# Performance work log

Hardware: AMD Instinct MI355X
Metric: run time of the kernel (lower is better)

## Reference

```python
import jax, jax.numpy as jnp
import numpy as np

B, S, HID = 4, 1024, 1024
NH, HD = 16, 64  # num heads, head dim


def setup_inputs() -> dict:
    key = jax.random.key(0)
    ks = jax.random.split(key, 8)
    scale = 0.02
    return {
        "hidden_states": jax.random.normal(ks[0], (B, S, HID), dtype=jnp.float32),
        "attention_mask": jnp.ones((B, 1, 1, S), dtype=jnp.float32),
        "Wq": jax.random.normal(ks[1], (HID, HID), dtype=jnp.float32) * scale,
        "bq": jnp.zeros((HID,), dtype=jnp.float32),
        "Wk": jax.random.normal(ks[2], (HID, HID), dtype=jnp.float32) * scale,
        "bk": jnp.zeros((HID,), dtype=jnp.float32),
        "Wv": jax.random.normal(ks[3], (HID, HID), dtype=jnp.float32) * scale,
        "bv": jnp.zeros((HID,), dtype=jnp.float32),
    }


def reference(hidden_states, attention_mask, Wq, bq, Wk, bk, Wv, bv):
    # Linear projections: torch nn.Linear computes x @ W.T + b
    q = hidden_states @ Wq.T + bq  # [B,S,HID]
    k = hidden_states @ Wk.T + bk
    v = hidden_states @ Wv.T + bv

    def split_heads(x):
        return x.reshape(B, S, NH, HD).transpose(0, 2, 1, 3)  # [B,NH,S,HD]

    q, k, v = split_heads(q), split_heads(k), split_heads(v)

    scores = jnp.einsum("bhqd,bhkd->bhqk", q, k) / jnp.sqrt(jnp.float32(HD))
    # faithful to original: scores - (2 - mask) * 1e6
    scores = scores - (2.0 - attention_mask) * 1.0e6
    probs = jax.nn.softmax(scores, axis=-1)
    # dropout: eval mode -> identity
    ctx = jnp.einsum("bhqk,bhkd->bhqd", probs, v)  # [B,NH,S,HD]
    ctx = ctx.transpose(0, 2, 1, 3).reshape(B, S, HID)
    return ctx
```

## Files before the change

### kernel.cpp

```cpp
#include <hip/hip_runtime.h>
#include <math.h>

#define B_ 4
#define S_ 1024
#define HID_ 1024
#define NH_ 16
#define HD_ 64
#define NTOK (B_ * S_)

typedef __attribute__((ext_vector_type(4))) float f32x4;
typedef __attribute__((ext_vector_type(16))) float f32x16;
typedef __attribute__((ext_vector_type(8))) short bf16x8;

__device__ __forceinline__ unsigned short f2bf(float f) {
    union { float f; unsigned int u; } v; v.f = f;
    unsigned int r = v.u + 0x7fffu + ((v.u >> 16) & 1u);
    return (unsigned short)(r >> 16);
}

#if __has_builtin(__builtin_amdgcn_cvt_pk_bf16_f32)
__device__ __forceinline__ unsigned int pk_bf16(float a, float b) {
    auto v = __builtin_amdgcn_cvt_pk_bf16_f32(a, b);
    union { decltype(v) v; unsigned int u; } cv; cv.v = v;
    return cv.u;
}
#else
__device__ __forceinline__ unsigned int pk_bf16(float a, float b) {
    return (unsigned int)f2bf(a) | ((unsigned int)f2bf(b) << 16);
}
#endif

#if __has_builtin(__builtin_amdgcn_permlane32_swap)
__device__ __forceinline__ void plswap(unsigned &a, unsigned &b) {
    typedef __attribute__((ext_vector_type(2))) int v2i;
    v2i r = __builtin_amdgcn_permlane32_swap((int)a, (int)b, false, false);
    a = (unsigned)r[0]; b = (unsigned)r[1];
}
#else
__device__ __forceinline__ void plswap(unsigned &a, unsigned &b) {
    const unsigned bl = __shfl_xor(b, 32);
    const unsigned ah = __shfl_xor(a, 32);
    const bool hi = ((threadIdx.x & 63) >> 5) != 0;
    const unsigned na = hi ? bl : a;
    const unsigned nb = hi ? b  : ah;
    a = na; b = nb;
}
#endif

__device__ __forceinline__ void load_lds16(const void* g, void* l) {
    __builtin_amdgcn_global_load_lds(
        (const __attribute__((address_space(1))) unsigned int*)(uintptr_t)g,
        (__attribute__((address_space(3))) unsigned int*)(uintptr_t)l,
        16, 0, 0);
}

__global__ __launch_bounds__(256) void cvt_all(
    const float* __restrict__ x, const float* __restrict__ wq,
    const float* __restrict__ wk, const float* __restrict__ wv,
    unsigned short* __restrict__ xb, unsigned short* __restrict__ wqb,
    unsigned short* __restrict__ wkb, unsigned short* __restrict__ wvb)
{
    const int which = blockIdx.y;
    const float* src = which == 0 ? x : which == 1 ? wq : which == 2 ? wk : wv;
    unsigned short* dst = which == 0 ? xb : which == 1 ? wqb : which == 2 ? wkb : wvb;
    const int n4 = (which == 0) ? (NTOK * HID_ / 4) : (HID_ * HID_ / 4);
    int i = blockIdx.x * 256 + threadIdx.x;
    if (i < n4) {
        float4 f = ((const float4*)src)[i];
        uint2 o;
        o.x = pk_bf16(f.x, f.y);
        o.y = pk_bf16(f.z, f.w);
        ((uint2*)dst)[i] = o;
    }
}

__global__ __launch_bounds__(512, 6) void qkv_gemm_mfma(
    const unsigned short* __restrict__ xb,
    const unsigned short* __restrict__ Wqb, const float* __restrict__ bq,
    const unsigned short* __restrict__ Wkb, const float* __restrict__ bk,
    const unsigned short* __restrict__ Wvb, const float* __restrict__ bv,
    unsigned short* __restrict__ qout, unsigned short* __restrict__ kout,
    unsigned short* __restrict__ vtout)
{
    const int which = blockIdx.z;
    const unsigned short* __restrict__ W = which == 0 ? Wqb : which == 1 ? Wkb : Wvb;
    const float* __restrict__ bias       = which == 0 ? bq  : which == 1 ? bk  : bv;

    __shared__ unsigned short As[128 * 64];
    __shared__ unsigned short Bs[128 * 64];

    const int t    = threadIdx.x;
    const int lane = t & 63;
    const int w    = t >> 6;
    const int wr   = w >> 2;
    const int wc   = w & 3;
    const int g    = lane >> 4;
    const int lrow = lane & 15;

    const int bm = blockIdx.x;
    const int bn = blockIdx.y;

    const unsigned short* __restrict__ Arow = (which == 2) ? W  : xb;
    const unsigned short* __restrict__ Brow = (which == 2) ? xb : W;
    const int am0 = (which == 2) ? bn * 128 : bm * 128;
    const int bn0 = (which == 2) ? bm * 128 : bn * 128;

    const int srow = t >> 3;
    const int sc   = ((t & 7) ^ ((t >> 3) & 7)) << 3;
    const unsigned short* gA = Arow + (size_t)(am0 + srow) * HID_ + sc;
    const unsigned short* gB = Brow + (size_t)(bn0 + srow) * HID_ + sc;

    const f32x4 zero = {0.f, 0.f, 0.f, 0.f};
    f32x4 acc[4][2];
    #pragma unroll
    for (int i = 0; i < 4; ++i)
        #pragma unroll
        for (int j = 0; j < 2; ++j) acc[i][j] = zero;

    for (int k0 = 0; k0 < HID_; k0 += 64) {
        __syncthreads();
        #pragma unroll
        for (int i = 0; i < 2; ++i) {
            load_lds16(gA + (size_t)(i * 64) * HID_ + k0, (char*)As + i * 8192 + t * 16);
            load_lds16(gB + (size_t)(i * 64) * HID_ + k0, (char*)Bs + i * 8192 + t * 16);
        }
        __syncthreads();

        #pragma unroll
        for (int ks = 0; ks < 2; ++ks) {
            bf16x8 af[4], bf[2];
            #pragma unroll
            for (int i = 0; i < 4; ++i) {
                const int row = wr * 64 + i * 16 + lrow;
                af[i] = *(const bf16x8*)&As[row * 64 + (((ks * 4 + g) ^ (row & 7)) << 3)];
            }
            #pragma unroll
            for (int j = 0; j < 2; ++j) {
                const int row = wc * 32 + j * 16 + lrow;
                bf[j] = *(const bf16x8*)&Bs[row * 64 + (((ks * 4 + g) ^ (row & 7)) << 3)];
            }
            #pragma unroll
            for (int i = 0; i < 4; ++i)
                #pragma unroll
                for (int j = 0; j < 2; ++j)
                    acc[i][j] = __builtin_amdgcn_mfma_f32_16x16x32_bf16(
                        af[i], bf[j], acc[i][j], 0, 0, 0);
        }
    }

    const int col   = lane & 15;
    const int rbase = (lane >> 4) << 2;
    if (which == 2) {
        #pragma unroll
        for (int i = 0; i < 4; ++i) {
            #pragma unroll
            for (int r = 0; r < 4; ++r) {
                const int feat = bn * 128 + wr * 64 + i * 16 + rbase + r;
                const int h = feat >> 6, d = feat & 63;
                const float bias_v = bias[feat];
                #pragma unroll
                for (int j = 0; j < 2; ++j) {
                    const int tok = bm * 128 + wc * 32 + j * 16 + col;
                    const int b = tok >> 10, s = tok & 1023;
                    vtout[((size_t)((b << 4) + h) << 16) + ((size_t)d << 10) + s] =
                        f2bf(acc[i][j][r] + bias_v);
                }
            }
        }
    } else {
        #pragma unroll
        for (int j = 0; j < 2; ++j) {
            const int feat = bn * 128 + wc * 32 + j * 16 + col;
            const int h = feat >> 6, d = feat & 63;
            const float bias_v = bias[feat];
            #pragma unroll
            for (int i = 0; i < 4; ++i) {
                const int tok0 = bm * 128 + wr * 64 + i * 16 + rbase;
                #pragma unroll
                for (int r = 0; r < 4; ++r) {
                    const int tok = tok0 + r;
                    const int b = tok >> 10, s = tok & 1023;
                    const size_t off = ((size_t)((b << 4) + h) << 16) + ((size_t)s << 6) + d;
                    const float val = acc[i][j][r] + bias_v;
                    if (which == 0) qout[off] = f2bf(val);
                    else            kout[off] = f2bf(val);
                }
            }
        }
    }
}

__global__ __launch_bounds__(256, 2) void attn_mfma(
    const unsigned short* __restrict__ Q, const unsigned short* __restrict__ K,
    const unsigned short* __restrict__ Vt, const float* __restrict__ mask,
    float* __restrict__ out)
{
    __shared__ unsigned short Ks[2][64 * 64];
    __shared__ unsigned short Vts[2][64 * 64];
    __shared__ float Mts[1024];
    __shared__ float Ls[4][32];

    const int t    = threadIdx.x;
    const int lane = t & 63;
    const int w    = t >> 6;
    const int q31  = lane & 31;
    const int hl   = lane >> 5;

    const int bh = blockIdx.x;
    const int b  = bh >> 4;
    const int h  = bh & 15;
    const int q0w = (blockIdx.y << 7) + (w << 5);

    const unsigned short* __restrict__ qg = Q  + ((size_t)bh << 16);
    const unsigned short* __restrict__ kg = K  + ((size_t)bh << 16);
    const unsigned short* __restrict__ vg = Vt + ((size_t)bh << 16);

    bf16x8 qreg[4];
    {
        const unsigned short* qp = qg + ((size_t)(q0w + q31) << 6);
        #pragma unroll
        for (int kc = 0; kc < 4; ++kc)
            qreg[kc] = *(const bf16x8*)&qp[kc * 16 + (hl << 3)];
    }

    int fro[4];
    #pragma unroll
    for (int kc = 0; kc < 4; ++kc)
        fro[kc] = q31 * 128 + ((((kc << 1) + hl) ^ (q31 & 7)) << 4);

    const int srow = t >> 3;
    const int c8   = ((t & 7) ^ (srow & 7)) << 3;
    const unsigned short* kst = kg + (size_t)srow * 64 + c8;
    const unsigned short* vst = vg + (size_t)srow * 1024 + c8;

    f32x16 O[2];
    #pragma unroll
    for (int i = 0; i < 16; ++i) { O[0][i] = 0.f; O[1][i] = 0.f; }
    float lacc = 0.f;

    #pragma unroll
    for (int i = 0; i < 2; ++i) {
        load_lds16(kst + i * 2048,  (char*)Ks[0]  + i * 4096 + t * 16);
        load_lds16(vst + i * 32768, (char*)Vts[0] + i * 4096 + t * 16);
    }
    #pragma unroll
    for (int i = 0; i < 4; ++i) {
        const int key = t + i * 256;
        Mts[key] = (2.0f - mask[(b << 10) + key]) * 1.0e6f;
    }
    __syncthreads();

    for (int kt = 0; kt < 16; ++kt) {
        const int cur = kt & 1;

        if (kt < 15) {
            #pragma unroll
            for (int i = 0; i < 2; ++i) {
                load_lds16(kst + i * 2048 + (size_t)(kt + 1) * 4096,
                           (char*)Ks[cur ^ 1] + i * 4096 + t * 16);
                load_lds16(vst + i * 32768 + (size_t)(kt + 1) * 64,
                           (char*)Vts[cur ^ 1] + i * 4096 + t * 16);
            }
        }

        const char* Kb = (const char*)Ks[cur];
        const char* Vb = (const char*)Vts[cur];

        f32x16 sacc[2];
        #pragma unroll
        for (int i = 0; i < 16; ++i) { sacc[0][i] = 0.f; sacc[1][i] = 0.f; }
        #pragma unroll
        for (int kb = 0; kb < 2; ++kb) {
            bf16x8 kf[4];
            #pragma unroll
            for (int kc = 0; kc < 4; ++kc)
                kf[kc] = *(const bf16x8*)(Kb + kb * 4096 + fro[kc]);
            __builtin_amdgcn_s_setprio(1);
            #pragma unroll
            for (int kc = 0; kc < 4; ++kc)
                sacc[kb] = __builtin_amdgcn_mfma_f32_32x32x16_bf16(
                    kf[kc], qreg[kc], sacc[kb], 0, 0, 0);
            __builtin_amdgcn_s_setprio(0);
        }

        bf16x8 pf[4];
        #pragma unroll
        for (int kb = 0; kb < 2; ++kb) {
            unsigned u[4][2];
            #pragma unroll
            for (int rq = 0; rq < 4; ++rq) {
                const f32x4 m4 = *(const f32x4*)&Mts[kt * 64 + kb * 32 + rq * 8 + (hl << 2)];
                float p[4];
                #pragma unroll
                for (int r = 0; r < 4; ++r) {
                    const float sv = sacc[kb][rq * 4 + r] * 0.125f - m4[r];
                    p[r] = __expf(sv + 1.0e6f);
                }
                lacc += (p[0] + p[1]) + (p[2] + p[3]);
                u[rq][0] = pk_bf16(p[0], p[1]);
                u[rq][1] = pk_bf16(p[2], p[3]);
            }
            #pragma unroll
            for (int c = 0; c < 2; ++c) {
                unsigned w0 = u[2 * c][0], w2 = u[2 * c + 1][0];
                plswap(w0, w2);
                unsigned w1 = u[2 * c][1], w3 = u[2 * c + 1][1];
                plswap(w1, w3);
                union { unsigned u[4]; bf16x8 v; } f;
                f.u[0] = w0; f.u[1] = w1; f.u[2] = w2; f.u[3] = w3;
                pf[kb * 2 + c] = f.v;
            }
        }

        #pragma unroll
        for (int hb = 0; hb < 2; ++hb) {
            bf16x8 vf[4];
            #pragma unroll
            for (int kc = 0; kc < 4; ++kc)
                vf[kc] = *(const bf16x8*)(Vb + hb * 4096 + fro[kc]);
            __builtin_amdgcn_s_setprio(1);
            #pragma unroll
            for (int kc = 0; kc < 4; ++kc)
                O[hb] = __builtin_amdgcn_mfma_f32_32x32x16_bf16(
                    pf[kc], vf[kc], O[hb], 0, 0, 0);
            __builtin_amdgcn_s_setprio(0);
        }

        __syncthreads();
    }

    const float l = lacc + __shfl_xor(lacc, 32);
    if (lane < 32) Ls[w][q31] = l;
    asm volatile("s_waitcnt lgkmcnt(0)" ::: "memory");
    #pragma unroll
    for (int r = 0; r < 16; ++r) {
        const int qr = (r & 3) + ((r >> 2) << 3) + (hl << 2);
        const float inv = 1.0f / Ls[w][qr];
        const size_t base = (((size_t)(b << 10) + (q0w + qr)) << 10) + (h << 6);
        out[base + q31]      = O[0][r] * inv;
        out[base + 32 + q31] = O[1][r] * inv;
    }
}

extern "C" void kernel_launch(void* const* d_in, const int* in_sizes, int n_in,
                              void* d_out, int out_size, void* d_ws, size_t ws_size,
                              hipStream_t stream) {
    const float* hs   = (const float*)d_in[0];
    const float* mask = (const float*)d_in[1];
    const float* Wq   = (const float*)d_in[2];
    const float* bq   = (const float*)d_in[3];
    const float* Wk   = (const float*)d_in[4];
    const float* bk   = (const float*)d_in[5];
    const float* Wv   = (const float*)d_in[6];
    const float* bv   = (const float*)d_in[7];
    float* out = (float*)d_out;

    char* ws = (char*)d_ws;
    unsigned short* xb  = (unsigned short*)(ws);
    unsigned short* wqb = (unsigned short*)(ws + ((size_t)8  << 20));
    unsigned short* wkb = (unsigned short*)(ws + ((size_t)10 << 20));
    unsigned short* wvb = (unsigned short*)(ws + ((size_t)12 << 20));
    unsigned short* qb  = (unsigned short*)(ws + ((size_t)14 << 20));
    unsigned short* kb  = (unsigned short*)(ws + ((size_t)22 << 20));
    unsigned short* vtb = (unsigned short*)(ws + ((size_t)30 << 20));

    cvt_all<<<dim3(4096, 4), 256, 0, stream>>>(hs, Wq, Wk, Wv, xb, wqb, wkb, wvb);
    qkv_gemm_mfma<<<dim3(NTOK / 128, HID_ / 128, 3), 512, 0, stream>>>(
        xb, wqb, bq, wkb, bk, wvb, bv, qb, kb, vtb);
    attn_mfma<<<dim3(B_ * NH_, S_ / 128), 256, 0, stream>>>(qb, kb, vtb, mask, out);
}
```

Baseline: 150.4 us.

## Split attention over two key halves and add a partial-sum combine kernel

The attention kernel gains a third grid dimension that splits the 1024 keys into two halves. Each block writes its unnormalized output and row sums to workspace, and a new combine kernel adds the two halves and normalizes. This doubles the block count and raises the launch-bounds occupancy target to 4, so more wavefronts are available to hide latency. In exchange it writes and re-reads about 32MB of fp32 partials and adds a kernel launch. The higher occupancy target may also force register spills.

```diff
diff --git a/kernel.cpp b/kernel.cpp
--- a/kernel.cpp
+++ b/kernel.cpp
@@ -190,15 +190,14 @@
     }
 }
 
-__global__ __launch_bounds__(256, 2) void attn_mfma(
+__global__ __launch_bounds__(256, 4) void attn_mfma(
     const unsigned short* __restrict__ Q, const unsigned short* __restrict__ K,
     const unsigned short* __restrict__ Vt, const float* __restrict__ mask,
-    float* __restrict__ out)
+    float* __restrict__ Opart, float* __restrict__ lpart)
 {
     __shared__ unsigned short Ks[2][64 * 64];
     __shared__ unsigned short Vts[2][64 * 64];
-    __shared__ float Mts[1024];
-    __shared__ float Ls[4][32];
+    __shared__ float Mts[512];
 
     const int t    = threadIdx.x;
     const int lane = t & 63;
@@ -210,6 +209,7 @@
     const int b  = bh >> 4;
     const int h  = bh & 15;
     const int q0w = (blockIdx.y << 7) + (w << 5);
+    const int kb0 = blockIdx.z << 9;
 
     const unsigned short* __restrict__ qg = Q  + ((size_t)bh << 16);
     const unsigned short* __restrict__ kg = K  + ((size_t)bh << 16);
@@ -230,8 +230,8 @@
 
     const int srow = t >> 3;
     const int c8   = ((t & 7) ^ (srow & 7)) << 3;
-    const unsigned short* kst = kg + (size_t)srow * 64 + c8;
-    const unsigned short* vst = vg + (size_t)srow * 1024 + c8;
+    const unsigned short* kst = kg + (size_t)(kb0 + srow) * 64 + c8;
+    const unsigned short* vst = vg + (size_t)srow * 1024 + kb0 + c8;
 
     f32x16 O[2];
     #pragma unroll
@@ -244,16 +244,16 @@
         load_lds16(vst + i * 32768, (char*)Vts[0] + i * 4096 + t * 16);
     }
     #pragma unroll
-    for (int i = 0; i < 4; ++i) {
+    for (int i = 0; i < 2; ++i) {
         const int key = t + i * 256;
-        Mts[key] = (2.0f - mask[(b << 10) + key]) * 1.0e6f;
+        Mts[key] = (2.0f - mask[(b << 10) + kb0 + key]) * 1.0e6f;
     }
     __syncthreads();
 
-    for (int kt = 0; kt < 16; ++kt) {
+    for (int kt = 0; kt < 8; ++kt) {
         const int cur = kt & 1;
 
-        if (kt < 15) {
+        if (kt < 7) {
             #pragma unroll
             for (int i = 0; i < 2; ++i) {
                 load_lds16(kst + i * 2048 + (size_t)(kt + 1) * 4096,
@@ -330,16 +330,37 @@
     }
 
     const float l = lacc + __shfl_xor(lacc, 32);
-    if (lane < 32) Ls[w][q31] = l;
-    asm volatile("s_waitcnt lgkmcnt(0)" ::: "memory");
+    if (lane < 32)
+        lpart[(((size_t)blockIdx.z << 6) + bh) * 1024 + q0w + q31] = l;
+    float* op = Opart + ((size_t)blockIdx.z << 22);
     #pragma unroll
     for (int r = 0; r < 16; ++r) {
         const int qr = (r & 3) + ((r >> 2) << 3) + (hl << 2);
-        const float inv = 1.0f / Ls[w][qr];
         const size_t base = (((size_t)(b << 10) + (q0w + qr)) << 10) + (h << 6);
-        out[base + q31]      = O[0][r] * inv;
-        out[base + 32 + q31] = O[1][r] * inv;
-    }
+        op[base + q31]      = O[0][r];
+        op[base + 32 + q31] = O[1][r];
+    }
+}
+
+__global__ __launch_bounds__(256) void attn_combine(
+    const float* __restrict__ Opart, const float* __restrict__ lpart,
+    float* __restrict__ out)
+{
+    const int i = blockIdx.x * 256 + threadIdx.x;
+    const int f4 = i << 2;
+    const int tok = f4 >> 10;
+    const int hid = f4 & 1023;
+    const int bh  = ((tok >> 10) << 4) + (hid >> 6);
+    const int q   = tok & 1023;
+
+    const float l = lpart[bh * 1024 + q] + lpart[(64 * 1024) + bh * 1024 + q];
+    const float inv = 1.0f / l;
+    const f32x4 o0 = *(const f32x4*)&Opart[f4];
+    const f32x4 o1 = *(const f32x4*)&Opart[(1 << 22) + f4];
+    f32x4 o;
+    #pragma unroll
+    for (int k = 0; k < 4; ++k) o[k] = (o0[k] + o1[k]) * inv;
+    *(f32x4*)&out[f4] = o;
 }
 
 extern "C" void kernel_launch(void* const* d_in, const int* in_sizes, int n_in,
@@ -363,9 +384,13 @@
     unsigned short* qb  = (unsigned short*)(ws + ((size_t)14 << 20));
     unsigned short* kb  = (unsigned short*)(ws + ((size_t)22 << 20));
     unsigned short* vtb = (unsigned short*)(ws + ((size_t)30 << 20));
+    float* Opart = (float*)(ws + ((size_t)40 << 20));
+    float* lpart = (float*)(ws + ((size_t)72 << 20));
 
     cvt_all<<<dim3(4096, 4), 256, 0, stream>>>(hs, Wq, Wk, Wv, xb, wqb, wkb, wvb);
     qkv_gemm_mfma<<<dim3(NTOK / 128, HID_ / 128, 3), 512, 0, stream>>>(
         xb, wqb, bq, wkb, bk, wvb, bv, qb, kb, vtb);
-    attn_mfma<<<dim3(B_ * NH_, S_ / 128), 256, 0, stream>>>(qb, kb, vtb, mask, out);
-}
+    attn_mfma<<<dim3(B_ * NH_, S_ / 128, 2), 256, 0, stream>>>(
+        qb, kb, vtb, mask, Opart, lpart);
+    attn_combine<<<dim3(NTOK * HID_ / 4 / 256), 256, 0, stream>>>(Opart, lpart, out);
+}
```

Result: no change. 152.9 us (+1.7%).
